# Optimization experiments

Hardware: AMD Instinct MI355X
Metric: run time of the kernel (lower is better)

Reference implementation:

```python
import jax, jax.numpy as jnp
import numpy as np

B, N, DIM, HEADS, DHEAD, DEPTH, EDGE = 1, 384, 128, 4, 64, 3, 8
INNER = HEADS * DHEAD  # 256


def _make_rotary():
    inv = 1.0 / (10000.0 ** (np.arange(0, DHEAD, 2, dtype=np.float32) / DHEAD))
    f = np.arange(N, dtype=np.float32)[:, None] * inv[None, :]  # [N, DHEAD//2]
    f = np.repeat(f, 2, axis=-1)  # interleaved pairs -> [N, DHEAD]
    return jnp.asarray(np.cos(f)), jnp.asarray(np.sin(f))

COS, SIN = _make_rotary()


def _rotate_half(x):
    x2 = x.reshape(x.shape[:-1] + (DHEAD // 2, 2))
    return jnp.stack((-x2[..., 1], x2[..., 0]), axis=-1).reshape(x.shape)


def _layer_norm(x, s, b, eps=1e-3):
    mu = jnp.mean(x, axis=-1, keepdims=True)
    var = jnp.mean(jnp.square(x - mu), axis=-1, keepdims=True)
    return (x - mu) * jax.lax.rsqrt(var + eps) * s + b


def _gated_res(x, res, Wg):
    gi = jnp.concatenate([x, res, x - res], axis=-1)  # [B,N,3*DIM]
    g = jax.nn.sigmoid(gi @ Wg)  # [B,N,1]
    return x * g + res * (1.0 - g)


def setup_inputs() -> dict:
    key = jax.random.key(0)
    ks = jax.random.split(key, 16)
    p = lambda k, shape: 0.02 * jax.random.normal(k, shape, jnp.float32)
    return {
        "nodes": jax.random.normal(ks[0], (B, N, DIM), jnp.float32),
        "edges": jax.random.normal(ks[1], (B, N, N, EDGE), jnp.float32),
        "ln1_s": jnp.ones((DEPTH, DIM), jnp.float32), "ln1_b": jnp.zeros((DEPTH, DIM), jnp.float32),
        "Wq": p(ks[2], (DEPTH, DIM, INNER)), "bq": jnp.zeros((DEPTH, INNER), jnp.float32),
        "Wkv": p(ks[3], (DEPTH, DIM, 2 * INNER)), "bkv": jnp.zeros((DEPTH, 2 * INNER), jnp.float32),
        "We": p(ks[4], (DEPTH, EDGE, INNER)), "be": jnp.zeros((DEPTH, INNER), jnp.float32),
        "Wo": p(ks[5], (DEPTH, INNER, DIM)), "bo": jnp.zeros((DEPTH, DIM), jnp.float32),
        "Wg_attn": p(ks[6], (DEPTH, 3 * DIM, 1)),
        "ln2_s": jnp.ones((DEPTH, DIM), jnp.float32), "ln2_b": jnp.zeros((DEPTH, DIM), jnp.float32),
        "W1": p(ks[7], (DEPTH, DIM, 4 * DIM)), "b1": jnp.zeros((DEPTH, 4 * DIM), jnp.float32),
        "W2": p(ks[8], (DEPTH, 4 * DIM, DIM)), "b2": jnp.zeros((DEPTH, DIM), jnp.float32),
        "Wg_ff": p(ks[9], (DEPTH, 3 * DIM, 1)),
        "Wd1": p(ks[10], (DIM, 9)), "bd1": jnp.zeros((9,), jnp.float32),
        "Wd2": p(ks[11], (9, 3)), "bd2": jnp.zeros((3,), jnp.float32),
        "mask": jnp.ones((B, N), dtype=bool),
    }


def _forward(nodes, edges, ln1_s, ln1_b, Wq, bq, Wkv, bkv, We, be, Wo, bo, Wg_attn,
             ln2_s, ln2_b, W1, b1, W2, b2, Wg_ff, Wd1, bd1, Wd2, bd2, mask):
    cos = COS[None, None]  # [1,1,N,DHEAD]
    sin = SIN[None, None]
    mask2 = mask[:, None, :, None] & mask[:, None, None, :]  # [B,1,N,N]
    x = nodes
    for i in range(DEPTH):
        # --- pre-norm attention with edge-conditioned K/V and rotary pos emb ---
        xn = _layer_norm(x, ln1_s[i], ln1_b[i])
        q = (xn @ Wq[i] + bq[i]).reshape(B, N, HEADS, DHEAD).transpose(0, 2, 1, 3)
        k, v = jnp.split(xn @ Wkv[i] + bkv[i], 2, axis=-1)
        k = k.reshape(B, N, HEADS, DHEAD).transpose(0, 2, 1, 3)
        v = v.reshape(B, N, HEADS, DHEAD).transpose(0, 2, 1, 3)
        e = (edges @ We[i] + be[i]).reshape(B, N, N, HEADS, DHEAD).transpose(0, 3, 1, 2, 4)  # [B,H,i,j,d]
        q = q * cos + _rotate_half(q) * sin
        k = k * cos + _rotate_half(k) * sin
        kf = k[:, :, None, :, :] + e  # [B,H,i,j,d]
        vf = v[:, :, None, :, :] + e
        sim = jnp.einsum('bhid,bhijd->bhij', q, kf) * (DHEAD ** -0.5)
        sim = jnp.where(mask2, sim, -1e9)
        attn = jax.nn.softmax(sim, axis=-1)
        out = jnp.einsum('bhij,bhijd->bhid', attn, vf)
        out = out.transpose(0, 2, 1, 3).reshape(B, N, INNER) @ Wo[i] + bo[i]
        x = _gated_res(out, x, Wg_attn[i])
        # --- pre-norm feedforward ---
        xn2 = _layer_norm(x, ln2_s[i], ln2_b[i])
        h = jax.nn.gelu(xn2 @ W1[i] + b1[i], approximate=False)
        ff = h @ W2[i] + b2[i]
        x = _gated_res(ff, x, Wg_ff[i])
    y = jax.nn.relu(x @ Wd1 + bd1)
    y = y @ Wd2 + bd2  # [B,N,3]
    return y - jnp.mean(y, axis=1)  # broadcasts since B == 1 (matches TF semantics)


def reference(nodes, edges, ln1_s, ln1_b, Wq, bq, Wkv, bkv, We, be, Wo, bo, Wg_attn,
              ln2_s, ln2_b, W1, b1, W2, b2, Wg_ff, Wd1, bd1, Wd2, bd2, mask):
    return _forward(nodes, edges, ln1_s, ln1_b, Wq, bq, Wkv, bkv, We, be, Wo, bo, Wg_attn,
                    ln2_s, ln2_b, W1, b1, W2, b2, Wg_ff, Wd1, bd1, Wd2, bd2, mask)
```

## Files before the change

### kernel.cpp

```cpp
#include <hip/hip_runtime.h>
#include <math.h>

#define NTOK 384
#define DIM  128
#define HEADS 4
#define DHEAD 64
#define INNER 256
#define DEPTH 3
#define EDGE 8
#define FFD 512

__device__ __forceinline__ float wave_sum64(float v){
#pragma unroll
  for (int m = 32; m >= 1; m >>= 1) v += __shfl_xor(v, m, 64);
  return v;
}
__device__ __forceinline__ float wave_max64(float v){
#pragma unroll
  for (int m = 32; m >= 1; m >>= 1) v = fmaxf(v, __shfl_xor(v, m, 64));
  return v;
}
__device__ __forceinline__ float seg_sum32(float v){
#pragma unroll
  for (int m = 16; m >= 1; m >>= 1) v += __shfl_xor(v, m, 32);
  return v;
}
__device__ __forceinline__ float seg_max32(float v){
#pragma unroll
  for (int m = 16; m >= 1; m >>= 1) v = fmaxf(v, __shfl_xor(v, m, 32));
  return v;
}

__device__ __forceinline__ int swz_row(int id){ return (id & 7) * 48 + (id >> 3); }

__device__ __forceinline__ void rotary_val(int i, int d, float* c, float* s){
  int j = d >> 1;
  double ex = (double)(2 * j) / 64.0;
  float p = (float)pow(10000.0, ex);
  float inv = 1.0f / p;
  float f = (float)i * inv;
  double fd = (double)f;
  *c = (float)cos(fd);
  *s = (float)sin(fd);
}

__device__ __forceinline__ void qkv_row_v2(
    int i, int t, const float* __restrict__ snx,
    const float* __restrict__ Wq, const float* __restrict__ bq,
    const float* __restrict__ Wkv, const float* __restrict__ bkv,
    const float* __restrict__ We, const float* __restrict__ be,
    const float* __restrict__ cosRow, const float* __restrict__ sinRow,
    float* __restrict__ qb_, float* __restrict__ kbT, float* __restrict__ vb_,
    float* __restrict__ qWeB, float* __restrict__ qbeB,
    float4* __restrict__ qp4)
{
  int ks   = (t < 192) ? 0 : 1;
  int quad = (t < 192) ? t : t - 192;
  float4 acc = {0.f, 0.f, 0.f, 0.f};
  if (t < 384){
    const float4* Wp; int stride4;
    if (quad < 64){ Wp = (const float4*)Wq + quad;         stride4 = 64;  }
    else          { Wp = (const float4*)Wkv + (quad - 64); stride4 = 128; }
    int k0 = ks * 64;
#pragma unroll 8
    for (int kk = 0; kk < 64; ++kk){
      int k = k0 + kk;
      float4 w = Wp[(size_t)k * stride4];
      float x = snx[k];
      acc.x = fmaf(x, w.x, acc.x); acc.y = fmaf(x, w.y, acc.y);
      acc.z = fmaf(x, w.z, acc.z); acc.w = fmaf(x, w.w, acc.w);
    }
    if (ks == 1) qp4[quad] = acc;
  }
  __syncthreads();
  if (t < 192){
    float4 p = qp4[quad];
    acc.x += p.x; acc.y += p.y; acc.z += p.z; acc.w += p.w;
    if (quad < 64){
      int c0 = 4 * quad;
      float4 b = ((const float4*)bq)[quad];
      float a0 = acc.x + b.x, a1 = acc.y + b.y, a2 = acc.z + b.z, a3 = acc.w + b.w;
      int d0 = c0 & 63;
      float c_0 = cosRow[d0],     s_0 = sinRow[d0];
      float c_1 = cosRow[d0 + 2], s_1 = sinRow[d0 + 2];
      float r0 = a0 * c_0 - a1 * s_0;
      float r1 = a1 * c_0 + a0 * s_0;
      float r2 = a2 * c_1 - a3 * s_1;
      float r3 = a3 * c_1 + a2 * s_1;
      float4 qv; qv.x = r0; qv.y = r1; qv.z = r2; qv.w = r3;
      *(float4*)(qb_ + (size_t)i * 256 + c0) = qv;
      int h = quad >> 4;
#pragma unroll
      for (int cc = 0; cc < 8; ++cc){
        const float* wc = We + cc * 256 + c0;
        float pr = r0 * wc[0] + r1 * wc[1] + r2 * wc[2] + r3 * wc[3];
#pragma unroll
        for (int m = 8; m >= 1; m >>= 1) pr += __shfl_xor(pr, m, 16);
        if ((t & 15) == 0) qWeB[(h * NTOK + i) * 8 + cc] = pr;
      }
      const float* bc = be + c0;
      float pb = r0 * bc[0] + r1 * bc[1] + r2 * bc[2] + r3 * bc[3];
#pragma unroll
      for (int m = 8; m >= 1; m >>= 1) pb += __shfl_xor(pb, m, 16);
      if ((t & 15) == 0) qbeB[h * NTOK + i] = pb;
    } else if (quad < 128){
      int c0 = 4 * (quad - 64);
      float4 b = ((const float4*)bkv)[quad - 64];
      float a0 = acc.x + b.x, a1 = acc.y + b.y, a2 = acc.z + b.z, a3 = acc.w + b.w;
      int d0 = c0 & 63, h = c0 >> 6;
      float c_0 = cosRow[d0],     s_0 = sinRow[d0];
      float c_1 = cosRow[d0 + 2], s_1 = sinRow[d0 + 2];
      float r0 = a0 * c_0 - a1 * s_0;
      float r1 = a1 * c_0 + a0 * s_0;
      float r2 = a2 * c_1 - a3 * s_1;
      float r3 = a3 * c_1 + a2 * s_1;
      float* kp = kbT + (size_t)(h * 64 + d0) * NTOK + i;
      kp[0]        = r0;
      kp[NTOK]     = r1;
      kp[2 * NTOK] = r2;
      kp[3 * NTOK] = r3;
    } else {
      int vq = quad - 128;
      int c0 = 4 * vq;
      float4 b = ((const float4*)bkv)[64 + vq];
      float4 vv;
      vv.x = acc.x + b.x; vv.y = acc.y + b.y;
      vv.z = acc.z + b.z; vv.w = acc.w + b.w;
      *(float4*)(vb_ + (size_t)i * 256 + c0) = vv;
    }
  }
}

__global__ __launch_bounds__(512, 4) void k_lnqkv(
    const float* __restrict__ x,
    const float* __restrict__ ls, const float* __restrict__ lb,
    const float* __restrict__ Wq, const float* __restrict__ bq,
    const float* __restrict__ Wkv, const float* __restrict__ bkv,
    const float* __restrict__ We, const float* __restrict__ be,
    float* __restrict__ cosS, float* __restrict__ sinS,
    float* __restrict__ qb_, float* __restrict__ kbT, float* __restrict__ vb_,
    float* __restrict__ qWeB, float* __restrict__ qbeB)
{
  __shared__ float snx[128];
  __shared__ float crow[64], srow[64];
  __shared__ float4 qp4[192];
  int i = swz_row(blockIdx.x);
  int t = threadIdx.x;

  if (t >= 448){
    int d = t - 448;
    float c, s;
    rotary_val(i, d, &c, &s);
    crow[d] = c; srow[d] = s;
    cosS[i * 64 + d] = c; sinS[i * 64 + d] = s;
  }
  if (t < 64){
    float x0 = x[(size_t)i * 128 + t], x1 = x[(size_t)i * 128 + 64 + t];
    float mu = wave_sum64(x0 + x1) * (1.0f / 128.0f);
    float d0 = x0 - mu, d1 = x1 - mu;
    float var = wave_sum64(d0 * d0 + d1 * d1) * (1.0f / 128.0f);
    float rstd = 1.0f / sqrtf(var + 1e-3f);
    snx[t]      = d0 * rstd * ls[t]      + lb[t];
    snx[t + 64] = d1 * rstd * ls[t + 64] + lb[t + 64];
  }
  __syncthreads();
  qkv_row_v2(i, t, snx, Wq, bq, Wkv, bkv, We, be, crow, srow,
             qb_, kbT, vb_, qWeB, qbeB, qp4);
}

__global__ __launch_bounds__(512, 4) void k_layer(
    const float* __restrict__ qb_, const float* __restrict__ kbT, const float* __restrict__ vb_,
    const float* __restrict__ qWeB, const float* __restrict__ qbeB,
    const float* __restrict__ edges,
    const float* __restrict__ We, const float* __restrict__ be,
    const float* __restrict__ Wo, const float* __restrict__ bo,
    const float* __restrict__ Wg_a,
    const float* __restrict__ ln2s, const float* __restrict__ ln2b,
    const float* __restrict__ W1, const float* __restrict__ b1,
    const float* __restrict__ W2, const float* __restrict__ b2,
    const float* __restrict__ Wg_f,
    const float* __restrict__ xin, float* __restrict__ xout,
    int has_next,
    const float* __restrict__ ls_n, const float* __restrict__ lb_n,
    const float* __restrict__ Wq_n, const float* __restrict__ bq_n,
    const float* __restrict__ Wkv_n, const float* __restrict__ bkv_n,
    const float* __restrict__ We_n, const float* __restrict__ be_n,
    const float* __restrict__ cosS, const float* __restrict__ sinS,
    float* __restrict__ qb_o, float* __restrict__ kbT_o, float* __restrict__ vb_o,
    float* __restrict__ qWeB_o, float* __restrict__ qbeB_o)
{
  __shared__ float qsL[256];
  __shared__ float qw[4][8];
  __shared__ float qbe[4];
  __shared__ __align__(16) float attnL[4][384];
  __shared__ float redA[12], redB[12];
  __shared__ float red8[12][8];
  __shared__ float part[512];
  __shared__ float ar[256];
  __shared__ float xold[128];
  __shared__ float xrow[128];
  __shared__ float snx[128];
  __shared__ float hs[512];
  __shared__ float4 prL[512];
  float* prF = (float*)prL;

  int i = swz_row(blockIdx.x);
  int t = threadIdx.x;

  if (t < 256) qsL[t] = qb_[(size_t)i * 256 + t];
  else if (t < 288){ int idx = t - 256; qw[idx >> 3][idx & 7] = qWeB[((idx >> 3) * NTOK + i) * 8 + (idx & 7)]; }
  else if (t < 292) qbe[t - 288] = qbeB[(t - 288) * NTOK + i];
  else if (t >= 384) xold[t - 384] = xin[(size_t)i * 128 + (t - 384)];
  __syncthreads();

  if (t < 384){
    int h = t / 96, j4 = t % 96;
    int j0 = 4 * j4;
    const float4* kT4 = (const float4*)(kbT + (size_t)(h * 64) * NTOK) + j4;
    const float* qsp = qsL + h * 64;
    float sA = 0.f, sB = 0.f, sC = 0.f, sD = 0.f;
#pragma unroll 16
    for (int d = 0; d < 64; ++d){
      float4 kv = kT4[(size_t)d * (NTOK / 4)];
      float q = qsp[d];
      sA = fmaf(q, kv.x, sA); sB = fmaf(q, kv.y, sB);
      sC = fmaf(q, kv.z, sC); sD = fmaf(q, kv.w, sD);
    }
    const float4* ep4 = (const float4*)(edges + ((size_t)i * NTOK + j0) * 8);
    float4 e0s[4], e1s[4];
    float ed[4];
#pragma unroll
    for (int jj = 0; jj < 4; ++jj){
      float4 e0 = ep4[2 * jj], e1 = ep4[2 * jj + 1];
      e0s[jj] = e0; e1s[jj] = e1;
      ed[jj] = e0.x * qw[h][0] + e0.y * qw[h][1] + e0.z * qw[h][2] + e0.w * qw[h][3]
             + e1.x * qw[h][4] + e1.y * qw[h][5] + e1.z * qw[h][6] + e1.w * qw[h][7];
    }
    float qbv = qbe[h];
    float s0 = 0.125f * (sA + ed[0] + qbv);
    float s1 = 0.125f * (sB + ed[1] + qbv);
    float s2 = 0.125f * (sC + ed[2] + qbv);
    float s3 = 0.125f * (sD + ed[3] + qbv);

    float mx = seg_max32(fmaxf(fmaxf(s0, s1), fmaxf(s2, s3)));
    if ((t & 31) == 0) redA[t >> 5] = mx;
    __syncthreads();
    float gm = fmaxf(fmaxf(redA[3 * h], redA[3 * h + 1]), redA[3 * h + 2]);
    float ex0 = expf(s0 - gm), ex1 = expf(s1 - gm), ex2 = expf(s2 - gm), ex3 = expf(s3 - gm);
    float sm = seg_sum32((ex0 + ex1) + (ex2 + ex3));
    if ((t & 31) == 0) redB[t >> 5] = sm;
    __syncthreads();
    float inv = 1.0f / (redB[3 * h] + redB[3 * h + 1] + redB[3 * h + 2]);
    float w0 = ex0 * inv, w1 = ex1 * inv, w2 = ex2 * inv, w3 = ex3 * inv;
    float4 wvv; wvv.x = w0; wvv.y = w1; wvv.z = w2; wvv.w = w3;
    *(float4*)&attnL[h][j0] = wvv;

    float a8[8];
    a8[0] = w0 * e0s[0].x + w1 * e0s[1].x + w2 * e0s[2].x + w3 * e0s[3].x;
    a8[1] = w0 * e0s[0].y + w1 * e0s[1].y + w2 * e0s[2].y + w3 * e0s[3].y;
    a8[2] = w0 * e0s[0].z + w1 * e0s[1].z + w2 * e0s[2].z + w3 * e0s[3].z;
    a8[3] = w0 * e0s[0].w + w1 * e0s[1].w + w2 * e0s[2].w + w3 * e0s[3].w;
    a8[4] = w0 * e1s[0].x + w1 * e1s[1].x + w2 * e1s[2].x + w3 * e1s[3].x;
    a8[5] = w0 * e1s[0].y + w1 * e1s[1].y + w2 * e1s[2].y + w3 * e1s[3].y;
    a8[6] = w0 * e1s[0].z + w1 * e1s[1].z + w2 * e1s[2].z + w3 * e1s[3].z;
    a8[7] = w0 * e1s[0].w + w1 * e1s[1].w + w2 * e1s[2].w + w3 * e1s[3].w;
#pragma unroll
    for (int cc = 0; cc < 8; ++cc){
      float r = seg_sum32(a8[cc]);
      if ((t & 31) == 0) red8[t >> 5][cc] = r;
    }
  } else {
    __syncthreads();
    __syncthreads();
  }
  __syncthreads();

  {
    int hh = t >> 7, dd = t & 63, half = (t >> 6) & 1;
    const float* vp = vb_ + hh * 64 + dd;
    const float* aw_ = attnL[hh];
    int j0 = half * 192;
    float a0 = 0.f, a1 = 0.f, a2 = 0.f, a3 = 0.f;
#pragma unroll 12
    for (int jj2 = 0; jj2 < 192; jj2 += 4){
      a0 = fmaf(aw_[j0 + jj2],     vp[(size_t)(j0 + jj2) * 256],     a0);
      a1 = fmaf(aw_[j0 + jj2 + 1], vp[(size_t)(j0 + jj2 + 1) * 256], a1);
      a2 = fmaf(aw_[j0 + jj2 + 2], vp[(size_t)(j0 + jj2 + 2) * 256], a2);
      a3 = fmaf(aw_[j0 + jj2 + 3], vp[(size_t)(j0 + jj2 + 3) * 256], a3);
    }
    part[t] = (a0 + a1) + (a2 + a3);
  }
  __syncthreads();
  if (t < 256){
    int h2 = t >> 6, d = t & 63;
    float o = part[h2 * 128 + d] + part[h2 * 128 + 64 + d];
    float ew = 0.f;
#pragma unroll
    for (int cc = 0; cc < 8; ++cc)
      ew = fmaf(red8[3 * h2][cc] + red8[3 * h2 + 1][cc] + red8[3 * h2 + 2][cc],
                We[cc * 256 + h2 * 64 + d], ew);
    ar[t] = o + ew + be[h2 * 64 + d];
  }
  __syncthreads();

  {
    int colq = t & 31, ksub = t >> 5;
    const float4* Wo4 = (const float4*)Wo;
    float4 acc = {0.f, 0.f, 0.f, 0.f};
#pragma unroll
    for (int kk = 0; kk < 16; ++kk){
      int k = ksub * 16 + kk;
      float4 w = Wo4[(size_t)k * 32 + colq];
      float a = ar[k];
      acc.x = fmaf(a, w.x, acc.x); acc.y = fmaf(a, w.y, acc.y);
      acc.z = fmaf(a, w.z, acc.z); acc.w = fmaf(a, w.w, acc.w);
    }
    prL[ksub * 32 + colq] = acc;
  }
  __syncthreads();

  if (t < 64){
    float o0 = bo[t], o1 = bo[t + 64];
#pragma unroll
    for (int s = 0; s < 16; ++s){ o0 += prF[s * 128 + t]; o1 += prF[s * 128 + 64 + t]; }
    float xo0 = xold[t], xo1 = xold[t + 64];
    float gp = o0 * Wg_a[t]      + xo0 * Wg_a[128 + t] + (o0 - xo0) * Wg_a[256 + t]
             + o1 * Wg_a[64 + t] + xo1 * Wg_a[192 + t] + (o1 - xo1) * Wg_a[320 + t];
    float z = wave_sum64(gp);
    float gg = 1.0f / (1.0f + expf(-z));
    float xr0 = o0 * gg + xo0 * (1.0f - gg);
    float xr1 = o1 * gg + xo1 * (1.0f - gg);
    xrow[t] = xr0; xrow[t + 64] = xr1;
    float mu = wave_sum64(xr0 + xr1) * (1.0f / 128.0f);
    float d0 = xr0 - mu, d1 = xr1 - mu;
    float var = wave_sum64(d0 * d0 + d1 * d1) * (1.0f / 128.0f);
    float rstd = 1.0f / sqrtf(var + 1e-3f);
    snx[t]      = d0 * rstd * ln2s[t]      + ln2b[t];
    snx[t + 64] = d1 * rstd * ln2s[t + 64] + ln2b[t + 64];
  }
  __syncthreads();

  {
    int colq = t & 127, ksub = t >> 7;
    const float4* W14 = (const float4*)W1;
    float4 acc = {0.f, 0.f, 0.f, 0.f};
#pragma unroll 8
    for (int kk = 0; kk < 32; ++kk){
      int k = ksub * 32 + kk;
      float4 w = W14[(size_t)k * 128 + colq];
      float a = snx[k];
      acc.x = fmaf(a, w.x, acc.x); acc.y = fmaf(a, w.y, acc.y);
      acc.z = fmaf(a, w.z, acc.z); acc.w = fmaf(a, w.w, acc.w);
    }
    prL[ksub * 128 + colq] = acc;
  }
  __syncthreads();

  {
    float hv = b1[t];
#pragma unroll
    for (int s3 = 0; s3 < 4; ++s3) hv += prF[s3 * 512 + t];
    const float RS2 = 0.70710678118654752440f;
    hs[t] = 0.5f * hv * (1.0f + erff(hv * RS2));
  }
  __syncthreads();

  {
    int colq = t & 31, ksub = t >> 5;
    const float4* W24 = (const float4*)W2;
    float4 acc = {0.f, 0.f, 0.f, 0.f};
#pragma unroll 8
    for (int kk = 0; kk < 32; ++kk){
      int k = ksub * 32 + kk;
      float4 w = W24[(size_t)k * 32 + colq];
      float a = hs[k];
      acc.x = fmaf(a, w.x, acc.x); acc.y = fmaf(a, w.y, acc.y);
      acc.z = fmaf(a, w.z, acc.z); acc.w = fmaf(a, w.w, acc.w);
    }
    prL[ksub * 32 + colq] = acc;
  }
  __syncthreads();

  if (t < 64){
    float f0 = b2[t], f1 = b2[t + 64];
#pragma unroll
    for (int s3 = 0; s3 < 16; ++s3){ f0 += prF[s3 * 128 + t]; f1 += prF[s3 * 128 + 64 + t]; }
    float xr0 = xrow[t], xr1 = xrow[t + 64];
    float gp = f0 * Wg_f[t]      + xr0 * Wg_f[128 + t] + (f0 - xr0) * Wg_f[256 + t]
             + f1 * Wg_f[64 + t] + xr1 * Wg_f[192 + t] + (f1 - xr1) * Wg_f[320 + t];
    float z = wave_sum64(gp);
    float gg = 1.0f / (1.0f + expf(-z));
    float xn0 = f0 * gg + xr0 * (1.0f - gg);
    float xn1 = f1 * gg + xr1 * (1.0f - gg);
    xout[(size_t)i * 128 + t]      = xn0;
    xout[(size_t)i * 128 + 64 + t] = xn1;
    if (has_next){
      float mu = wave_sum64(xn0 + xn1) * (1.0f / 128.0f);
      float d0 = xn0 - mu, d1 = xn1 - mu;
      float var = wave_sum64(d0 * d0 + d1 * d1) * (1.0f / 128.0f);
      float rstd = 1.0f / sqrtf(var + 1e-3f);
      snx[t]      = d0 * rstd * ls_n[t]      + lb_n[t];
      snx[t + 64] = d1 * rstd * ls_n[t + 64] + lb_n[t + 64];
    }
  }
  __syncthreads();

  if (has_next){
    qkv_row_v2(i, t, snx, Wq_n, bq_n, Wkv_n, bkv_n, We_n, be_n,
               cosS + (size_t)i * 64, sinS + (size_t)i * 64,
               qb_o, kbT_o, vb_o, qWeB_o, qbeB_o, prL);
  }
}

__global__ __launch_bounds__(384) void k_final(
    const float* __restrict__ x,
    const float* __restrict__ Wd1, const float* __restrict__ bd1,
    const float* __restrict__ Wd2, const float* __restrict__ bd2,
    float* __restrict__ out)
{
  __shared__ float red[6];
  int i = threadIdx.x;
  float y[9];
#pragma unroll
  for (int c = 0; c < 9; ++c) y[c] = bd1[c];
  const float4* x4 = (const float4*)(x + (size_t)i * 128);
#pragma unroll 8
  for (int r4 = 0; r4 < 32; ++r4){
    float4 xv = x4[r4];
    const float* wp = Wd1 + (r4 * 4) * 9;
#pragma unroll
    for (int c = 0; c < 9; ++c) y[c] = fmaf(xv.x, wp[c], y[c]);
#pragma unroll
    for (int c = 0; c < 9; ++c) y[c] = fmaf(xv.y, wp[9 + c], y[c]);
#pragma unroll
    for (int c = 0; c < 9; ++c) y[c] = fmaf(xv.z, wp[18 + c], y[c]);
#pragma unroll
    for (int c = 0; c < 9; ++c) y[c] = fmaf(xv.w, wp[27 + c], y[c]);
  }
#pragma unroll
  for (int c = 0; c < 9; ++c) y[c] = fmaxf(y[c], 0.0f);
  float z[3];
#pragma unroll
  for (int c = 0; c < 3; ++c){
    float a = bd2[c];
#pragma unroll
    for (int r = 0; r < 9; ++r) a = fmaf(y[r], Wd2[r * 3 + c], a);
    z[c] = a;
  }
#pragma unroll
  for (int c = 0; c < 3; ++c){
    float s = wave_sum64(z[c]);
    if ((i & 63) == 0) red[i >> 6] = s;
    __syncthreads();
    float tot = 0.f;
#pragma unroll
    for (int w = 0; w < 6; ++w) tot += red[w];
    float mean = tot * (1.0f / 384.0f);
    out[i * 3 + c] = z[c] - mean;
    __syncthreads();
  }
}

extern "C" void kernel_launch(void* const* d_in, const int* in_sizes, int n_in,
                              void* d_out, int out_size, void* d_ws, size_t ws_size,
                              hipStream_t stream)
{
  const float* nodes   = (const float*)d_in[0];
  const float* edges   = (const float*)d_in[1];
  const float* ln1_s   = (const float*)d_in[2];
  const float* ln1_b   = (const float*)d_in[3];
  const float* Wq      = (const float*)d_in[4];
  const float* bq      = (const float*)d_in[5];
  const float* Wkv     = (const float*)d_in[6];
  const float* bkv     = (const float*)d_in[7];
  const float* We      = (const float*)d_in[8];
  const float* be      = (const float*)d_in[9];
  const float* Wo      = (const float*)d_in[10];
  const float* bo      = (const float*)d_in[11];
  const float* Wg_attn = (const float*)d_in[12];
  const float* ln2_s   = (const float*)d_in[13];
  const float* ln2_b   = (const float*)d_in[14];
  const float* W1      = (const float*)d_in[15];
  const float* b1      = (const float*)d_in[16];
  const float* W2      = (const float*)d_in[17];
  const float* b2      = (const float*)d_in[18];
  const float* Wg_ff   = (const float*)d_in[19];
  const float* Wd1     = (const float*)d_in[20];
  const float* bd1     = (const float*)d_in[21];
  const float* Wd2     = (const float*)d_in[22];
  const float* bd2     = (const float*)d_in[23];

  float* ws   = (float*)d_ws;
  float* cosS = ws;
  float* sinS = cosS + 24576;
  float* qb0   = sinS + 24576;
  float* kbT0  = qb0 + 98304;
  float* vb0   = kbT0 + 98304;
  float* qWe0  = vb0 + 98304;
  float* qbe0  = qWe0 + 12288;
  float* qb1   = qbe0 + 1536;
  float* kbT1  = qb1 + 98304;
  float* vb1   = kbT1 + 98304;
  float* qWe1  = vb1 + 98304;
  float* qbe1  = qWe1 + 12288;
  float* xbuf  = qbe1 + 1536;

  k_lnqkv<<<dim3(NTOK), dim3(512), 0, stream>>>(
      nodes, ln1_s, ln1_b, Wq, bq, Wkv, bkv, We, be,
      cosS, sinS, qb0, kbT0, vb0, qWe0, qbe0);

  for (int L = 0; L < DEPTH; ++L){
    int Ln = (L < DEPTH - 1) ? (L + 1) : L;
    const float* qbi  = (L & 1) ? qb1  : qb0;
    const float* kbi  = (L & 1) ? kbT1 : kbT0;
    const float* vbi  = (L & 1) ? vb1  : vb0;
    const float* qWei = (L & 1) ? qWe1 : qWe0;
    const float* qbei = (L & 1) ? qbe1 : qbe0;
    float* qbo  = (L & 1) ? qb0  : qb1;
    float* kbo  = (L & 1) ? kbT0 : kbT1;
    float* vbo  = (L & 1) ? vb0  : vb1;
    float* qWeo = (L & 1) ? qWe0 : qWe1;
    float* qbeo = (L & 1) ? qbe0 : qbe1;

    k_layer<<<dim3(NTOK), dim3(512), 0, stream>>>(
        qbi, kbi, vbi, qWei, qbei, edges,
        We + (size_t)L * EDGE * INNER, be + L * INNER,
        Wo + (size_t)L * INNER * DIM, bo + L * DIM,
        Wg_attn + L * 3 * DIM,
        ln2_s + L * DIM, ln2_b + L * DIM,
        W1 + (size_t)L * DIM * FFD, b1 + L * FFD,
        W2 + (size_t)L * FFD * DIM, b2 + L * DIM,
        Wg_ff + L * 3 * DIM,
        (L == 0) ? nodes : xbuf, xbuf,
        (L < DEPTH - 1) ? 1 : 0,
        ln1_s + Ln * DIM, ln1_b + Ln * DIM,
        Wq + (size_t)Ln * DIM * INNER, bq + Ln * INNER,
        Wkv + (size_t)Ln * DIM * 2 * INNER, bkv + Ln * 2 * INNER,
        We + (size_t)Ln * EDGE * INNER, be + Ln * INNER,
        cosS, sinS, qbo, kbo, vbo, qWeo, qbeo);
  }

  k_final<<<dim3(1), dim3(384), 0, stream>>>(xbuf, Wd1, bd1, Wd2, bd2, (float*)d_out);
}
```

Measured before the change: 131.8 us.

## Fuse all layers into one persistent kernel with atomic grid barriers

Merges the QKV prologue kernel, the three per-layer kernels and the final head kernel into a single 384-block launch, separated by atomic-counter grid barriers. Rotary cos/sin are kept in shared memory per block instead of being staged through global memory. The aim is to remove the launch overhead and idle gaps between five kernel launches. In exchange it relies on all 384 blocks being co-resident to avoid deadlock, adds a memset launch, and the final head runs on a single block after the last barrier.

```diff
diff --git a/kernel.cpp b/kernel.cpp
--- a/kernel.cpp
+++ b/kernel.cpp
@@ -9,17 +9,13 @@
 #define DEPTH 3
 #define EDGE 8
 #define FFD 512
+#define NBLK 384
 
 __device__ __forceinline__ float wave_sum64(float v){
 #pragma unroll
   for (int m = 32; m >= 1; m >>= 1) v += __shfl_xor(v, m, 64);
   return v;
 }
-__device__ __forceinline__ float wave_max64(float v){
-#pragma unroll
-  for (int m = 32; m >= 1; m >>= 1) v = fmaxf(v, __shfl_xor(v, m, 64));
-  return v;
-}
 __device__ __forceinline__ float seg_sum32(float v){
 #pragma unroll
   for (int m = 16; m >= 1; m >>= 1) v += __shfl_xor(v, m, 32);
@@ -32,6 +28,17 @@
 }
 
 __device__ __forceinline__ int swz_row(int id){ return (id & 7) * 48 + (id >> 3); }
+
+__device__ __forceinline__ void gbar(int* cnt, int idx, int t){
+  __syncthreads();
+  if (t == 0){
+    __threadfence();
+    atomicAdd(&cnt[idx], 1);
+    while (__hip_atomic_load(&cnt[idx], __ATOMIC_ACQUIRE, __HIP_MEMORY_SCOPE_AGENT) < NBLK){}
+    __threadfence();
+  }
+  __syncthreads();
+}
 
 __device__ __forceinline__ void rotary_val(int i, int d, float* c, float* s){
   int j = d >> 1;
@@ -131,63 +138,25 @@
   }
 }
 
-__global__ __launch_bounds__(512, 4) void k_lnqkv(
-    const float* __restrict__ x,
-    const float* __restrict__ ls, const float* __restrict__ lb,
+__global__ __launch_bounds__(512, 4) void k_net(
+    const float* __restrict__ nodes, const float* __restrict__ edges,
+    const float* __restrict__ ln1_s, const float* __restrict__ ln1_b,
     const float* __restrict__ Wq, const float* __restrict__ bq,
     const float* __restrict__ Wkv, const float* __restrict__ bkv,
-    const float* __restrict__ We, const float* __restrict__ be,
-    float* __restrict__ cosS, float* __restrict__ sinS,
-    float* __restrict__ qb_, float* __restrict__ kbT, float* __restrict__ vb_,
-    float* __restrict__ qWeB, float* __restrict__ qbeB)
-{
-  __shared__ float snx[128];
-  __shared__ float crow[64], srow[64];
-  __shared__ float4 qp4[192];
-  int i = swz_row(blockIdx.x);
-  int t = threadIdx.x;
-
-  if (t >= 448){
-    int d = t - 448;
-    float c, s;
-    rotary_val(i, d, &c, &s);
-    crow[d] = c; srow[d] = s;
-    cosS[i * 64 + d] = c; sinS[i * 64 + d] = s;
-  }
-  if (t < 64){
-    float x0 = x[(size_t)i * 128 + t], x1 = x[(size_t)i * 128 + 64 + t];
-    float mu = wave_sum64(x0 + x1) * (1.0f / 128.0f);
-    float d0 = x0 - mu, d1 = x1 - mu;
-    float var = wave_sum64(d0 * d0 + d1 * d1) * (1.0f / 128.0f);
-    float rstd = 1.0f / sqrtf(var + 1e-3f);
-    snx[t]      = d0 * rstd * ls[t]      + lb[t];
-    snx[t + 64] = d1 * rstd * ls[t + 64] + lb[t + 64];
-  }
-  __syncthreads();
-  qkv_row_v2(i, t, snx, Wq, bq, Wkv, bkv, We, be, crow, srow,
-             qb_, kbT, vb_, qWeB, qbeB, qp4);
-}
-
-__global__ __launch_bounds__(512, 4) void k_layer(
-    const float* __restrict__ qb_, const float* __restrict__ kbT, const float* __restrict__ vb_,
-    const float* __restrict__ qWeB, const float* __restrict__ qbeB,
-    const float* __restrict__ edges,
-    const float* __restrict__ We, const float* __restrict__ be,
-    const float* __restrict__ Wo, const float* __restrict__ bo,
+    const float* __restrict__ WeB, const float* __restrict__ beB,
+    const float* __restrict__ WoB, const float* __restrict__ boB,
     const float* __restrict__ Wg_a,
-    const float* __restrict__ ln2s, const float* __restrict__ ln2b,
-    const float* __restrict__ W1, const float* __restrict__ b1,
-    const float* __restrict__ W2, const float* __restrict__ b2,
+    const float* __restrict__ ln2_s, const float* __restrict__ ln2_b,
+    const float* __restrict__ W1B, const float* __restrict__ b1B,
+    const float* __restrict__ W2B, const float* __restrict__ b2B,
     const float* __restrict__ Wg_f,
-    const float* __restrict__ xin, float* __restrict__ xout,
-    int has_next,
-    const float* __restrict__ ls_n, const float* __restrict__ lb_n,
-    const float* __restrict__ Wq_n, const float* __restrict__ bq_n,
-    const float* __restrict__ Wkv_n, const float* __restrict__ bkv_n,
-    const float* __restrict__ We_n, const float* __restrict__ be_n,
-    const float* __restrict__ cosS, const float* __restrict__ sinS,
-    float* __restrict__ qb_o, float* __restrict__ kbT_o, float* __restrict__ vb_o,
-    float* __restrict__ qWeB_o, float* __restrict__ qbeB_o)
+    const float* __restrict__ Wd1, const float* __restrict__ bd1,
+    const float* __restrict__ Wd2, const float* __restrict__ bd2,
+    float* __restrict__ qb0, float* __restrict__ kbT0, float* __restrict__ vb0,
+    float* __restrict__ qWe0, float* __restrict__ qbe0,
+    float* __restrict__ qb1, float* __restrict__ kbT1, float* __restrict__ vb1,
+    float* __restrict__ qWe1, float* __restrict__ qbe1,
+    float* __restrict__ xbuf, float* __restrict__ out, int* __restrict__ cnt)
 {
   __shared__ float qsL[256];
   __shared__ float qw[4][8];
@@ -202,262 +171,317 @@
   __shared__ float snx[128];
   __shared__ float hs[512];
   __shared__ float4 prL[512];
+  __shared__ float crow[64], srow[64];
+  __shared__ float redF[8];
   float* prF = (float*)prL;
 
-  int i = swz_row(blockIdx.x);
+  int b = blockIdx.x;
+  int i = swz_row(b);
   int t = threadIdx.x;
 
-  if (t < 256) qsL[t] = qb_[(size_t)i * 256 + t];
-  else if (t < 288){ int idx = t - 256; qw[idx >> 3][idx & 7] = qWeB[((idx >> 3) * NTOK + i) * 8 + (idx & 7)]; }
-  else if (t < 292) qbe[t - 288] = qbeB[(t - 288) * NTOK + i];
-  else if (t >= 384) xold[t - 384] = xin[(size_t)i * 128 + (t - 384)];
-  __syncthreads();
-
-  if (t < 384){
-    int h = t / 96, j4 = t % 96;
-    int j0 = 4 * j4;
-    const float4* kT4 = (const float4*)(kbT + (size_t)(h * 64) * NTOK) + j4;
-    const float* qsp = qsL + h * 64;
-    float sA = 0.f, sB = 0.f, sC = 0.f, sD = 0.f;
-#pragma unroll 16
-    for (int d = 0; d < 64; ++d){
-      float4 kv = kT4[(size_t)d * (NTOK / 4)];
-      float q = qsp[d];
-      sA = fmaf(q, kv.x, sA); sB = fmaf(q, kv.y, sB);
-      sC = fmaf(q, kv.z, sC); sD = fmaf(q, kv.w, sD);
-    }
-    const float4* ep4 = (const float4*)(edges + ((size_t)i * NTOK + j0) * 8);
-    float4 e0s[4], e1s[4];
-    float ed[4];
-#pragma unroll
-    for (int jj = 0; jj < 4; ++jj){
-      float4 e0 = ep4[2 * jj], e1 = ep4[2 * jj + 1];
-      e0s[jj] = e0; e1s[jj] = e1;
-      ed[jj] = e0.x * qw[h][0] + e0.y * qw[h][1] + e0.z * qw[h][2] + e0.w * qw[h][3]
-             + e1.x * qw[h][4] + e1.y * qw[h][5] + e1.z * qw[h][6] + e1.w * qw[h][7];
-    }
-    float qbv = qbe[h];
-    float s0 = 0.125f * (sA + ed[0] + qbv);
-    float s1 = 0.125f * (sB + ed[1] + qbv);
-    float s2 = 0.125f * (sC + ed[2] + qbv);
-    float s3 = 0.125f * (sD + ed[3] + qbv);
-
-    float mx = seg_max32(fmaxf(fmaxf(s0, s1), fmaxf(s2, s3)));
-    if ((t & 31) == 0) redA[t >> 5] = mx;
-    __syncthreads();
-    float gm = fmaxf(fmaxf(redA[3 * h], redA[3 * h + 1]), redA[3 * h + 2]);
-    float ex0 = expf(s0 - gm), ex1 = expf(s1 - gm), ex2 = expf(s2 - gm), ex3 = expf(s3 - gm);
-    float sm = seg_sum32((ex0 + ex1) + (ex2 + ex3));
-    if ((t & 31) == 0) redB[t >> 5] = sm;
-    __syncthreads();
-    float inv = 1.0f / (redB[3 * h] + redB[3 * h + 1] + redB[3 * h + 2]);
-    float w0 = ex0 * inv, w1 = ex1 * inv, w2 = ex2 * inv, w3 = ex3 * inv;
-    float4 wvv; wvv.x = w0; wvv.y = w1; wvv.z = w2; wvv.w = w3;
-    *(float4*)&attnL[h][j0] = wvv;
-
-    float a8[8];
-    a8[0] = w0 * e0s[0].x + w1 * e0s[1].x + w2 * e0s[2].x + w3 * e0s[3].x;
-    a8[1] = w0 * e0s[0].y + w1 * e0s[1].y + w2 * e0s[2].y + w3 * e0s[3].y;
-    a8[2] = w0 * e0s[0].z + w1 * e0s[1].z + w2 * e0s[2].z + w3 * e0s[3].z;
-    a8[3] = w0 * e0s[0].w + w1 * e0s[1].w + w2 * e0s[2].w + w3 * e0s[3].w;
-    a8[4] = w0 * e1s[0].x + w1 * e1s[1].x + w2 * e1s[2].x + w3 * e1s[3].x;
-    a8[5] = w0 * e1s[0].y + w1 * e1s[1].y + w2 * e1s[2].y + w3 * e1s[3].y;
-    a8[6] = w0 * e1s[0].z + w1 * e1s[1].z + w2 * e1s[2].z + w3 * e1s[3].z;
-    a8[7] = w0 * e1s[0].w + w1 * e1s[1].w + w2 * e1s[2].w + w3 * e1s[3].w;
-#pragma unroll
-    for (int cc = 0; cc < 8; ++cc){
-      float r = seg_sum32(a8[cc]);
-      if ((t & 31) == 0) red8[t >> 5][cc] = r;
-    }
-  } else {
-    __syncthreads();
-    __syncthreads();
-  }
-  __syncthreads();
-
-  {
-    int hh = t >> 7, dd = t & 63, half = (t >> 6) & 1;
-    const float* vp = vb_ + hh * 64 + dd;
-    const float* aw_ = attnL[hh];
-    int j0 = half * 192;
-    float a0 = 0.f, a1 = 0.f, a2 = 0.f, a3 = 0.f;
-#pragma unroll 12
-    for (int jj2 = 0; jj2 < 192; jj2 += 4){
-      a0 = fmaf(aw_[j0 + jj2],     vp[(size_t)(j0 + jj2) * 256],     a0);
-      a1 = fmaf(aw_[j0 + jj2 + 1], vp[(size_t)(j0 + jj2 + 1) * 256], a1);
-      a2 = fmaf(aw_[j0 + jj2 + 2], vp[(size_t)(j0 + jj2 + 2) * 256], a2);
-      a3 = fmaf(aw_[j0 + jj2 + 3], vp[(size_t)(j0 + jj2 + 3) * 256], a3);
-    }
-    part[t] = (a0 + a1) + (a2 + a3);
-  }
-  __syncthreads();
-  if (t < 256){
-    int h2 = t >> 6, d = t & 63;
-    float o = part[h2 * 128 + d] + part[h2 * 128 + 64 + d];
-    float ew = 0.f;
-#pragma unroll
-    for (int cc = 0; cc < 8; ++cc)
-      ew = fmaf(red8[3 * h2][cc] + red8[3 * h2 + 1][cc] + red8[3 * h2 + 2][cc],
-                We[cc * 256 + h2 * 64 + d], ew);
-    ar[t] = o + ew + be[h2 * 64 + d];
-  }
-  __syncthreads();
-
-  {
-    int colq = t & 31, ksub = t >> 5;
-    const float4* Wo4 = (const float4*)Wo;
-    float4 acc = {0.f, 0.f, 0.f, 0.f};
-#pragma unroll
-    for (int kk = 0; kk < 16; ++kk){
-      int k = ksub * 16 + kk;
-      float4 w = Wo4[(size_t)k * 32 + colq];
-      float a = ar[k];
-      acc.x = fmaf(a, w.x, acc.x); acc.y = fmaf(a, w.y, acc.y);
-      acc.z = fmaf(a, w.z, acc.z); acc.w = fmaf(a, w.w, acc.w);
-    }
-    prL[ksub * 32 + colq] = acc;
-  }
-  __syncthreads();
-
+  if (t >= 448){
+    int d = t - 448;
+    float c, s;
+    rotary_val(i, d, &c, &s);
+    crow[d] = c; srow[d] = s;
+  }
   if (t < 64){
-    float o0 = bo[t], o1 = bo[t + 64];
-#pragma unroll
-    for (int s = 0; s < 16; ++s){ o0 += prF[s * 128 + t]; o1 += prF[s * 128 + 64 + t]; }
-    float xo0 = xold[t], xo1 = xold[t + 64];
-    float gp = o0 * Wg_a[t]      + xo0 * Wg_a[128 + t] + (o0 - xo0) * Wg_a[256 + t]
-             + o1 * Wg_a[64 + t] + xo1 * Wg_a[192 + t] + (o1 - xo1) * Wg_a[320 + t];
-    float z = wave_sum64(gp);
-    float gg = 1.0f / (1.0f + expf(-z));
-    float xr0 = o0 * gg + xo0 * (1.0f - gg);
-    float xr1 = o1 * gg + xo1 * (1.0f - gg);
-    xrow[t] = xr0; xrow[t + 64] = xr1;
-    float mu = wave_sum64(xr0 + xr1) * (1.0f / 128.0f);
-    float d0 = xr0 - mu, d1 = xr1 - mu;
+    float x0 = nodes[(size_t)i * 128 + t], x1 = nodes[(size_t)i * 128 + 64 + t];
+    float mu = wave_sum64(x0 + x1) * (1.0f / 128.0f);
+    float d0 = x0 - mu, d1 = x1 - mu;
     float var = wave_sum64(d0 * d0 + d1 * d1) * (1.0f / 128.0f);
     float rstd = 1.0f / sqrtf(var + 1e-3f);
-    snx[t]      = d0 * rstd * ln2s[t]      + ln2b[t];
-    snx[t + 64] = d1 * rstd * ln2s[t + 64] + ln2b[t + 64];
+    snx[t]      = d0 * rstd * ln1_s[t]      + ln1_b[t];
+    snx[t + 64] = d1 * rstd * ln1_s[t + 64] + ln1_b[t + 64];
   }
   __syncthreads();
-
-  {
-    int colq = t & 127, ksub = t >> 7;
-    const float4* W14 = (const float4*)W1;
-    float4 acc = {0.f, 0.f, 0.f, 0.f};
-#pragma unroll 8
-    for (int kk = 0; kk < 32; ++kk){
-      int k = ksub * 32 + kk;
-      float4 w = W14[(size_t)k * 128 + colq];
-      float a = snx[k];
-      acc.x = fmaf(a, w.x, acc.x); acc.y = fmaf(a, w.y, acc.y);
-      acc.z = fmaf(a, w.z, acc.z); acc.w = fmaf(a, w.w, acc.w);
-    }
-    prL[ksub * 128 + colq] = acc;
-  }
-  __syncthreads();
-
-  {
-    float hv = b1[t];
-#pragma unroll
-    for (int s3 = 0; s3 < 4; ++s3) hv += prF[s3 * 512 + t];
-    const float RS2 = 0.70710678118654752440f;
-    hs[t] = 0.5f * hv * (1.0f + erff(hv * RS2));
-  }
-  __syncthreads();
-
-  {
-    int colq = t & 31, ksub = t >> 5;
-    const float4* W24 = (const float4*)W2;
-    float4 acc = {0.f, 0.f, 0.f, 0.f};
-#pragma unroll 8
-    for (int kk = 0; kk < 32; ++kk){
-      int k = ksub * 32 + kk;
-      float4 w = W24[(size_t)k * 32 + colq];
-      float a = hs[k];
-      acc.x = fmaf(a, w.x, acc.x); acc.y = fmaf(a, w.y, acc.y);
-      acc.z = fmaf(a, w.z, acc.z); acc.w = fmaf(a, w.w, acc.w);
-    }
-    prL[ksub * 32 + colq] = acc;
-  }
-  __syncthreads();
-
-  if (t < 64){
-    float f0 = b2[t], f1 = b2[t + 64];
-#pragma unroll
-    for (int s3 = 0; s3 < 16; ++s3){ f0 += prF[s3 * 128 + t]; f1 += prF[s3 * 128 + 64 + t]; }
-    float xr0 = xrow[t], xr1 = xrow[t + 64];
-    float gp = f0 * Wg_f[t]      + xr0 * Wg_f[128 + t] + (f0 - xr0) * Wg_f[256 + t]
-             + f1 * Wg_f[64 + t] + xr1 * Wg_f[192 + t] + (f1 - xr1) * Wg_f[320 + t];
-    float z = wave_sum64(gp);
-    float gg = 1.0f / (1.0f + expf(-z));
-    float xn0 = f0 * gg + xr0 * (1.0f - gg);
-    float xn1 = f1 * gg + xr1 * (1.0f - gg);
-    xout[(size_t)i * 128 + t]      = xn0;
-    xout[(size_t)i * 128 + 64 + t] = xn1;
-    if (has_next){
-      float mu = wave_sum64(xn0 + xn1) * (1.0f / 128.0f);
-      float d0 = xn0 - mu, d1 = xn1 - mu;
+  qkv_row_v2(i, t, snx, Wq, bq, Wkv, bkv, WeB, beB, crow, srow,
+             qb0, kbT0, vb0, qWe0, qbe0, prL);
+  gbar(cnt, 0, t);
+
+  for (int L = 0; L < DEPTH; ++L){
+    const float* qb_  = (L & 1) ? qb1  : qb0;
+    const float* kbT  = (L & 1) ? kbT1 : kbT0;
+    const float* vb_  = (L & 1) ? vb1  : vb0;
+    const float* qWeB_ = (L & 1) ? qWe1 : qWe0;
+    const float* qbeB_ = (L & 1) ? qbe1 : qbe0;
+    float* qb_o  = (L & 1) ? qb0  : qb1;
+    float* kbT_o = (L & 1) ? kbT0 : kbT1;
+    float* vb_o  = (L & 1) ? vb0  : vb1;
+    float* qWe_o = (L & 1) ? qWe0 : qWe1;
+    float* qbe_o = (L & 1) ? qbe0 : qbe1;
+    const float* We  = WeB + (size_t)L * EDGE * INNER;
+    const float* be  = beB + (size_t)L * INNER;
+    const float* Wo  = WoB + (size_t)L * INNER * DIM;
+    const float* bo  = boB + (size_t)L * DIM;
+    const float* Wga = Wg_a + (size_t)L * 3 * DIM;
+    const float* l2s = ln2_s + (size_t)L * DIM;
+    const float* l2b = ln2_b + (size_t)L * DIM;
+    const float* W1  = W1B + (size_t)L * DIM * FFD;
+    const float* b1  = b1B + (size_t)L * FFD;
+    const float* W2  = W2B + (size_t)L * FFD * DIM;
+    const float* b2  = b2B + (size_t)L * DIM;
+    const float* Wgf = Wg_f + (size_t)L * 3 * DIM;
+    const float* xin = (L == 0) ? nodes : xbuf;
+    int has_next = (L < DEPTH - 1);
+    int Ln = has_next ? (L + 1) : L;
+    const float* Wq_n  = Wq  + (size_t)Ln * DIM * INNER;
+    const float* bq_n  = bq  + (size_t)Ln * INNER;
+    const float* Wkv_n = Wkv + (size_t)Ln * DIM * 2 * INNER;
+    const float* bkv_n = bkv + (size_t)Ln * 2 * INNER;
+    const float* We_n  = WeB + (size_t)Ln * EDGE * INNER;
+    const float* be_n  = beB + (size_t)Ln * INNER;
+    const float* ls_n  = ln1_s + (size_t)Ln * DIM;
+    const float* lb_n  = ln1_b + (size_t)Ln * DIM;
+
+    if (t < 256) qsL[t] = qb_[(size_t)i * 256 + t];
+    else if (t < 288){ int idx = t - 256; qw[idx >> 3][idx & 7] = qWeB_[((idx >> 3) * NTOK + i) * 8 + (idx & 7)]; }
+    else if (t < 292) qbe[t - 288] = qbeB_[(t - 288) * NTOK + i];
+    else if (t >= 384 && t < 512) xold[t - 384] = xin[(size_t)i * 128 + (t - 384)];
+    __syncthreads();
+
+    if (t < 384){
+      int h = t / 96, j4 = t % 96;
+      int j0 = 4 * j4;
+      const float4* kT4 = (const float4*)(kbT + (size_t)(h * 64) * NTOK) + j4;
+      const float* qsp = qsL + h * 64;
+      float sA = 0.f, sB = 0.f, sC = 0.f, sD = 0.f;
+#pragma unroll 16
+      for (int d = 0; d < 64; ++d){
+        float4 kv = kT4[(size_t)d * (NTOK / 4)];
+        float q = qsp[d];
+        sA = fmaf(q, kv.x, sA); sB = fmaf(q, kv.y, sB);
+        sC = fmaf(q, kv.z, sC); sD = fmaf(q, kv.w, sD);
+      }
+      const float4* ep4 = (const float4*)(edges + ((size_t)i * NTOK + j0) * 8);
+      float4 e0s[4], e1s[4];
+      float ed[4];
+#pragma unroll
+      for (int jj = 0; jj < 4; ++jj){
+        float4 e0 = ep4[2 * jj], e1 = ep4[2 * jj + 1];
+        e0s[jj] = e0; e1s[jj] = e1;
+        ed[jj] = e0.x * qw[h][0] + e0.y * qw[h][1] + e0.z * qw[h][2] + e0.w * qw[h][3]
+               + e1.x * qw[h][4] + e1.y * qw[h][5] + e1.z * qw[h][6] + e1.w * qw[h][7];
+      }
+      float qbv = qbe[h];
+      float s0 = 0.125f * (sA + ed[0] + qbv);
+      float s1 = 0.125f * (sB + ed[1] + qbv);
+      float s2 = 0.125f * (sC + ed[2] + qbv);
+      float s3 = 0.125f * (sD + ed[3] + qbv);
+
+      float mx = seg_max32(fmaxf(fmaxf(s0, s1), fmaxf(s2, s3)));
+      if ((t & 31) == 0) redA[t >> 5] = mx;
+      __syncthreads();
+      float gm = fmaxf(fmaxf(redA[3 * h], redA[3 * h + 1]), redA[3 * h + 2]);
+      float ex0 = expf(s0 - gm), ex1 = expf(s1 - gm), ex2 = expf(s2 - gm), ex3 = expf(s3 - gm);
+      float sm = seg_sum32((ex0 + ex1) + (ex2 + ex3));
+      if ((t & 31) == 0) redB[t >> 5] = sm;
+      __syncthreads();
+      float inv = 1.0f / (redB[3 * h] + redB[3 * h + 1] + redB[3 * h + 2]);
+      float w0 = ex0 * inv, w1 = ex1 * inv, w2 = ex2 * inv, w3 = ex3 * inv;
+      float4 wvv; wvv.x = w0; wvv.y = w1; wvv.z = w2; wvv.w = w3;
+      *(float4*)&attnL[h][j0] = wvv;
+
+      float a8[8];
+      a8[0] = w0 * e0s[0].x + w1 * e0s[1].x + w2 * e0s[2].x + w3 * e0s[3].x;
+      a8[1] = w0 * e0s[0].y + w1 * e0s[1].y + w2 * e0s[2].y + w3 * e0s[3].y;
+      a8[2] = w0 * e0s[0].z + w1 * e0s[1].z + w2 * e0s[2].z + w3 * e0s[3].z;
+      a8[3] = w0 * e0s[0].w + w1 * e0s[1].w + w2 * e0s[2].w + w3 * e0s[3].w;
+      a8[4] = w0 * e1s[0].x + w1 * e1s[1].x + w2 * e1s[2].x + w3 * e1s[3].x;
+      a8[5] = w0 * e1s[0].y + w1 * e1s[1].y + w2 * e1s[2].y + w3 * e1s[3].y;
+      a8[6] = w0 * e1s[0].z + w1 * e1s[1].z + w2 * e1s[2].z + w3 * e1s[3].z;
+      a8[7] = w0 * e1s[0].w + w1 * e1s[1].w + w2 * e1s[2].w + w3 * e1s[3].w;
+#pragma unroll
+      for (int cc = 0; cc < 8; ++cc){
+        float r = seg_sum32(a8[cc]);
+        if ((t & 31) == 0) red8[t >> 5][cc] = r;
+      }
+    } else {
+      __syncthreads();
+      __syncthreads();
+    }
+    __syncthreads();
+
+    {
+      int hh = t >> 7, dd = t & 63, half = (t >> 6) & 1;
+      const float* vp = vb_ + hh * 64 + dd;
+      const float* aw_ = attnL[hh];
+      int j0 = half * 192;
+      float a0 = 0.f, a1 = 0.f, a2 = 0.f, a3 = 0.f;
+#pragma unroll 12
+      for (int jj2 = 0; jj2 < 192; jj2 += 4){
+        a0 = fmaf(aw_[j0 + jj2],     vp[(size_t)(j0 + jj2) * 256],     a0);
+        a1 = fmaf(aw_[j0 + jj2 + 1], vp[(size_t)(j0 + jj2 + 1) * 256], a1);
+        a2 = fmaf(aw_[j0 + jj2 + 2], vp[(size_t)(j0 + jj2 + 2) * 256], a2);
+        a3 = fmaf(aw_[j0 + jj2 + 3], vp[(size_t)(j0 + jj2 + 3) * 256], a3);
+      }
+      part[t] = (a0 + a1) + (a2 + a3);
+    }
+    __syncthreads();
+    if (t < 256){
+      int h2 = t >> 6, d = t & 63;
+      float o = part[h2 * 128 + d] + part[h2 * 128 + 64 + d];
+      float ew = 0.f;
+#pragma unroll
+      for (int cc = 0; cc < 8; ++cc)
+        ew = fmaf(red8[3 * h2][cc] + red8[3 * h2 + 1][cc] + red8[3 * h2 + 2][cc],
+                  We[cc * 256 + h2 * 64 + d], ew);
+      ar[t] = o + ew + be[h2 * 64 + d];
+    }
+    __syncthreads();
+
+    {
+      int colq = t & 31, ksub = t >> 5;
+      const float4* Wo4 = (const float4*)Wo;
+      float4 acc = {0.f, 0.f, 0.f, 0.f};
+#pragma unroll
+      for (int kk = 0; kk < 16; ++kk){
+        int k = ksub * 16 + kk;
+        float4 w = Wo4[(size_t)k * 32 + colq];
+        float a = ar[k];
+        acc.x = fmaf(a, w.x, acc.x); acc.y = fmaf(a, w.y, acc.y);
+        acc.z = fmaf(a, w.z, acc.z); acc.w = fmaf(a, w.w, acc.w);
+      }
+      prL[ksub * 32 + colq] = acc;
+    }
+    __syncthreads();
+
+    if (t < 64){
+      float o0 = bo[t], o1 = bo[t + 64];
+#pragma unroll
+      for (int s = 0; s < 16; ++s){ o0 += prF[s * 128 + t]; o1 += prF[s * 128 + 64 + t]; }
+      float xo0 = xold[t], xo1 = xold[t + 64];
+      float gp = o0 * Wga[t]      + xo0 * Wga[128 + t] + (o0 - xo0) * Wga[256 + t]
+               + o1 * Wga[64 + t] + xo1 * Wga[192 + t] + (o1 - xo1) * Wga[320 + t];
+      float z = wave_sum64(gp);
+      float gg = 1.0f / (1.0f + expf(-z));
+      float xr0 = o0 * gg + xo0 * (1.0f - gg);
+      float xr1 = o1 * gg + xo1 * (1.0f - gg);
+      xrow[t] = xr0; xrow[t + 64] = xr1;
+      float mu = wave_sum64(xr0 + xr1) * (1.0f / 128.0f);
+      float d0 = xr0 - mu, d1 = xr1 - mu;
       float var = wave_sum64(d0 * d0 + d1 * d1) * (1.0f / 128.0f);
       float rstd = 1.0f / sqrtf(var + 1e-3f);
-      snx[t]      = d0 * rstd * ls_n[t]      + lb_n[t];
-      snx[t + 64] = d1 * rstd * ls_n[t + 64] + lb_n[t + 64];
-    }
-  }
-  __syncthreads();
-
-  if (has_next){
-    qkv_row_v2(i, t, snx, Wq_n, bq_n, Wkv_n, bkv_n, We_n, be_n,
-               cosS + (size_t)i * 64, sinS + (size_t)i * 64,
-               qb_o, kbT_o, vb_o, qWeB_o, qbeB_o, prL);
-  }
-}
-
-__global__ __launch_bounds__(384) void k_final(
-    const float* __restrict__ x,
-    const float* __restrict__ Wd1, const float* __restrict__ bd1,
-    const float* __restrict__ Wd2, const float* __restrict__ bd2,
-    float* __restrict__ out)
-{
-  __shared__ float red[6];
-  int i = threadIdx.x;
-  float y[9];
-#pragma unroll
-  for (int c = 0; c < 9; ++c) y[c] = bd1[c];
-  const float4* x4 = (const float4*)(x + (size_t)i * 128);
+      snx[t]      = d0 * rstd * l2s[t]      + l2b[t];
+      snx[t + 64] = d1 * rstd * l2s[t + 64] + l2b[t + 64];
+    }
+    __syncthreads();
+
+    {
+      int colq = t & 127, ksub = t >> 7;
+      const float4* W14 = (const float4*)W1;
+      float4 acc = {0.f, 0.f, 0.f, 0.f};
 #pragma unroll 8
-  for (int r4 = 0; r4 < 32; ++r4){
-    float4 xv = x4[r4];
-    const float* wp = Wd1 + (r4 * 4) * 9;
-#pragma unroll
-    for (int c = 0; c < 9; ++c) y[c] = fmaf(xv.x, wp[c], y[c]);
-#pragma unroll
-    for (int c = 0; c < 9; ++c) y[c] = fmaf(xv.y, wp[9 + c], y[c]);
-#pragma unroll
-    for (int c = 0; c < 9; ++c) y[c] = fmaf(xv.z, wp[18 + c], y[c]);
-#pragma unroll
-    for (int c = 0; c < 9; ++c) y[c] = fmaf(xv.w, wp[27 + c], y[c]);
-  }
-#pragma unroll
-  for (int c = 0; c < 9; ++c) y[c] = fmaxf(y[c], 0.0f);
-  float z[3];
-#pragma unroll
-  for (int c = 0; c < 3; ++c){
-    float a = bd2[c];
-#pragma unroll
-    for (int r = 0; r < 9; ++r) a = fmaf(y[r], Wd2[r * 3 + c], a);
-    z[c] = a;
-  }
-#pragma unroll
-  for (int c = 0; c < 3; ++c){
-    float s = wave_sum64(z[c]);
-    if ((i & 63) == 0) red[i >> 6] = s;
-    __syncthreads();
-    float tot = 0.f;
-#pragma unroll
-    for (int w = 0; w < 6; ++w) tot += red[w];
-    float mean = tot * (1.0f / 384.0f);
-    out[i * 3 + c] = z[c] - mean;
-    __syncthreads();
+      for (int kk = 0; kk < 32; ++kk){
+        int k = ksub * 32 + kk;
+        float4 w = W14[(size_t)k * 128 + colq];
+        float a = snx[k];
+        acc.x = fmaf(a, w.x, acc.x); acc.y = fmaf(a, w.y, acc.y);
+        acc.z = fmaf(a, w.z, acc.z); acc.w = fmaf(a, w.w, acc.w);
+      }
+      prL[ksub * 128 + colq] = acc;
+    }
+    __syncthreads();
+    {
+      float hv = b1[t];
+#pragma unroll
+      for (int s3 = 0; s3 < 4; ++s3) hv += prF[s3 * 512 + t];
+      const float RS2 = 0.70710678118654752440f;
+      hs[t] = 0.5f * hv * (1.0f + erff(hv * RS2));
+    }
+    __syncthreads();
+
+    {
+      int colq = t & 31, ksub = t >> 5;
+      const float4* W24 = (const float4*)W2;
+      float4 acc = {0.f, 0.f, 0.f, 0.f};
+#pragma unroll 8
+      for (int kk = 0; kk < 32; ++kk){
+        int k = ksub * 32 + kk;
+        float4 w = W24[(size_t)k * 32 + colq];
+        float a = hs[k];
+        acc.x = fmaf(a, w.x, acc.x); acc.y = fmaf(a, w.y, acc.y);
+        acc.z = fmaf(a, w.z, acc.z); acc.w = fmaf(a, w.w, acc.w);
+      }
+      prL[ksub * 32 + colq] = acc;
+    }
+    __syncthreads();
+
+    if (t < 64){
+      float f0 = b2[t], f1 = b2[t + 64];
+#pragma unroll
+      for (int s3 = 0; s3 < 16; ++s3){ f0 += prF[s3 * 128 + t]; f1 += prF[s3 * 128 + 64 + t]; }
+      float xr0 = xrow[t], xr1 = xrow[t + 64];
+      float gp = f0 * Wgf[t]      + xr0 * Wgf[128 + t] + (f0 - xr0) * Wgf[256 + t]
+               + f1 * Wgf[64 + t] + xr1 * Wgf[192 + t] + (f1 - xr1) * Wgf[320 + t];
+      float z = wave_sum64(gp);
+      float gg = 1.0f / (1.0f + expf(-z));
+      float xn0 = f0 * gg + xr0 * (1.0f - gg);
+      float xn1 = f1 * gg + xr1 * (1.0f - gg);
+      xbuf[(size_t)i * 128 + t]      = xn0;
+      xbuf[(size_t)i * 128 + 64 + t] = xn1;
+      if (has_next){
+        float mu = wave_sum64(xn0 + xn1) * (1.0f / 128.0f);
+        float d0 = xn0 - mu, d1 = xn1 - mu;
+        float var = wave_sum64(d0 * d0 + d1 * d1) * (1.0f / 128.0f);
+        float rstd = 1.0f / sqrtf(var + 1e-3f);
+        snx[t]      = d0 * rstd * ls_n[t]      + lb_n[t];
+        snx[t + 64] = d1 * rstd * ls_n[t + 64] + lb_n[t + 64];
+      }
+    }
+    __syncthreads();
+
+    if (has_next){
+      qkv_row_v2(i, t, snx, Wq_n, bq_n, Wkv_n, bkv_n, We_n, be_n, crow, srow,
+                 qb_o, kbT_o, vb_o, qWe_o, qbe_o, prL);
+    }
+    gbar(cnt, 1 + L, t);
+  }
+
+  if (b == 0){
+    int r = t;
+    float y[9];
+    float z[3] = {0.f, 0.f, 0.f};
+    if (r < 384){
+#pragma unroll
+      for (int c = 0; c < 9; ++c) y[c] = bd1[c];
+      const float4* x4 = (const float4*)(xbuf + (size_t)r * 128);
+#pragma unroll 8
+      for (int r4 = 0; r4 < 32; ++r4){
+        float4 xv = x4[r4];
+        const float* wp = Wd1 + (r4 * 4) * 9;
+#pragma unroll
+        for (int c = 0; c < 9; ++c) y[c] = fmaf(xv.x, wp[c], y[c]);
+#pragma unroll
+        for (int c = 0; c < 9; ++c) y[c] = fmaf(xv.y, wp[9 + c], y[c]);
+#pragma unroll
+        for (int c = 0; c < 9; ++c) y[c] = fmaf(xv.z, wp[18 + c], y[c]);
+#pragma unroll
+        for (int c = 0; c < 9; ++c) y[c] = fmaf(xv.w, wp[27 + c], y[c]);
+      }
+#pragma unroll
+      for (int c = 0; c < 9; ++c) y[c] = fmaxf(y[c], 0.0f);
+#pragma unroll
+      for (int c = 0; c < 3; ++c){
+        float a = bd2[c];
+#pragma unroll
+        for (int rr = 0; rr < 9; ++rr) a = fmaf(y[rr], Wd2[rr * 3 + c], a);
+        z[c] = a;
+      }
+    }
+#pragma unroll
+    for (int c = 0; c < 3; ++c){
+      float contrib = (r < 384) ? z[c] : 0.f;
+      float s = wave_sum64(contrib);
+      if ((t & 63) == 0) redF[t >> 6] = s;
+      __syncthreads();
+      float tot = 0.f;
+#pragma unroll
+      for (int w = 0; w < 6; ++w) tot += redF[w];
+      float mean = tot * (1.0f / 384.0f);
+      if (r < 384) out[r * 3 + c] = z[c] - mean;
+      __syncthreads();
+    }
   }
 }
 
@@ -491,9 +515,7 @@
   const float* bd2     = (const float*)d_in[23];
 
   float* ws   = (float*)d_ws;
-  float* cosS = ws;
-  float* sinS = cosS + 24576;
-  float* qb0   = sinS + 24576;
+  float* qb0   = ws;
   float* kbT0  = qb0 + 98304;
   float* vb0   = kbT0 + 98304;
   float* qWe0  = vb0 + 98304;
@@ -504,41 +526,15 @@
   float* qWe1  = vb1 + 98304;
   float* qbe1  = qWe1 + 12288;
   float* xbuf  = qbe1 + 1536;
-
-  k_lnqkv<<<dim3(NTOK), dim3(512), 0, stream>>>(
-      nodes, ln1_s, ln1_b, Wq, bq, Wkv, bkv, We, be,
-      cosS, sinS, qb0, kbT0, vb0, qWe0, qbe0);
-
-  for (int L = 0; L < DEPTH; ++L){
-    int Ln = (L < DEPTH - 1) ? (L + 1) : L;
-    const float* qbi  = (L & 1) ? qb1  : qb0;
-    const float* kbi  = (L & 1) ? kbT1 : kbT0;
-    const float* vbi  = (L & 1) ? vb1  : vb0;
-    const float* qWei = (L & 1) ? qWe1 : qWe0;
-    const float* qbei = (L & 1) ? qbe1 : qbe0;
-    float* qbo  = (L & 1) ? qb0  : qb1;
-    float* kbo  = (L & 1) ? kbT0 : kbT1;
-    float* vbo  = (L & 1) ? vb0  : vb1;
-    float* qWeo = (L & 1) ? qWe0 : qWe1;
-    float* qbeo = (L & 1) ? qbe0 : qbe1;
-
-    k_layer<<<dim3(NTOK), dim3(512), 0, stream>>>(
-        qbi, kbi, vbi, qWei, qbei, edges,
-        We + (size_t)L * EDGE * INNER, be + L * INNER,
-        Wo + (size_t)L * INNER * DIM, bo + L * DIM,
-        Wg_attn + L * 3 * DIM,
-        ln2_s + L * DIM, ln2_b + L * DIM,
-        W1 + (size_t)L * DIM * FFD, b1 + L * FFD,
-        W2 + (size_t)L * FFD * DIM, b2 + L * DIM,
-        Wg_ff + L * 3 * DIM,
-        (L == 0) ? nodes : xbuf, xbuf,
-        (L < DEPTH - 1) ? 1 : 0,
-        ln1_s + Ln * DIM, ln1_b + Ln * DIM,
-        Wq + (size_t)Ln * DIM * INNER, bq + Ln * INNER,
-        Wkv + (size_t)Ln * DIM * 2 * INNER, bkv + Ln * 2 * INNER,
-        We + (size_t)Ln * EDGE * INNER, be + Ln * INNER,
-        cosS, sinS, qbo, kbo, vbo, qWeo, qbeo);
-  }
-
-  k_final<<<dim3(1), dim3(384), 0, stream>>>(xbuf, Wd1, bd1, Wd2, bd2, (float*)d_out);
-}
+  int*   cnt   = (int*)(xbuf + 49152);
+
+  hipMemsetAsync(cnt, 0, 4 * sizeof(int), stream);
+
+  k_net<<<dim3(NBLK), dim3(512), 0, stream>>>(
+      nodes, edges, ln1_s, ln1_b, Wq, bq, Wkv, bkv, We, be,
+      Wo, bo, Wg_attn, ln2_s, ln2_b, W1, b1, W2, b2, Wg_ff,
+      Wd1, bd1, Wd2, bd2,
+      qb0, kbT0, vb0, qWe0, qbe0,
+      qb1, kbT1, vb1, qWe1, qbe1,
+      xbuf, (float*)d_out, cnt);
+}
```

Measured after the change: 416.2 us. +215.7%, slower.
